# Kernel tuning notes

Measured on AMD Instinct MI355X. Metric: run time of the kernel, lower is better.

The kernel has to match this reference:

```python
import jax, jax.numpy as jnp
import numpy as np

N = 100_000   # num destination nodes (adj rows)
M = 100_000   # num source/neighbor nodes (adj cols)
E = 3_200_000 # num edges (avg degree 32)
D_IN = 128
DIM = 128
LEAKY_ALPHA = 0.2  # tf.nn.leaky_relu default


def setup_inputs() -> dict:
    key = jax.random.key(0)
    ks = jax.random.split(key, 7)
    return {
        "self_embedding": jax.random.normal(ks[0], (N, D_IN), jnp.float32),
        "neigh_embedding": jax.random.normal(ks[1], (M, D_IN), jnp.float32),
        "W": jax.random.normal(ks[2], (D_IN, DIM), jnp.float32) / np.sqrt(D_IN).astype(np.float32),
        "w_self": jax.random.normal(ks[3], (DIM, 1), jnp.float32) * 0.1,
        "w_neigh": jax.random.normal(ks[4], (DIM, 1), jnp.float32) * 0.1,
        "edge_row": jax.random.randint(ks[5], (E,), 0, N, jnp.int32),
        "edge_col": jax.random.randint(ks[6], (E,), 0, M, jnp.int32),
    }


def reference(self_embedding, neigh_embedding, W, w_self, w_neigh, edge_row, edge_col):
    # Dense projections (shared weight, no bias)
    from_all = neigh_embedding @ W    # [M, DIM]
    from_self = self_embedding @ W    # [N, DIM]

    # Per-node attention logits
    self_weight = (from_self @ w_self)[:, 0]   # [N]
    all_weight = (from_all @ w_neigh)[:, 0]    # [M]

    # Per-edge score: leaky_relu(self_weight[row] + all_weight[col])
    scores = jax.nn.leaky_relu(self_weight[edge_row] + all_weight[edge_col],
                               negative_slope=LEAKY_ALPHA)  # [E]

    n = self_embedding.shape[0]
    # Sparse (segment) softmax over each row's edges, numerically stable
    row_max = jax.ops.segment_max(scores, edge_row, num_segments=n)
    row_max = jnp.where(jnp.isfinite(row_max), row_max, 0.0)  # guard empty rows
    e = jnp.exp(scores - row_max[edge_row])
    denom = jax.ops.segment_sum(e, edge_row, num_segments=n)
    denom = jnp.where(denom > 0, denom, 1.0)
    alpha = e / denom[edge_row]  # [E]

    # Sparse-dense matmul: output[i] = sum_j alpha_ij * from_all[j]
    agg = jax.ops.segment_sum(alpha[:, None] * from_all[edge_col], edge_row,
                              num_segments=n)  # [N, DIM]

    # renorm=False path: residual with from_self, then activation
    return jax.nn.relu(from_self + agg)
```

## Files before the change

### kernel.cpp

```cpp
#include <hip/hip_runtime.h>
#include <math.h>

#define DIM 128
#define LEAKY 0.2f
#define CAP 80
#define RPB 128
#define NBMAX 1024
#define PART_CHUNK 4096

typedef __attribute__((ext_vector_type(8))) short short8_t;
typedef __attribute__((ext_vector_type(8))) __bf16 bf16x8;
typedef __attribute__((ext_vector_type(4))) float f32x4;

__device__ __forceinline__ unsigned short f32_to_bf16_bits(float x) {
  unsigned u = __float_as_uint(x);
  u += 0x7fffu + ((u >> 16) & 1u);
  return (unsigned short)(u >> 16);
}

__global__ __launch_bounds__(256) void gemm_neigh_q(
    const float* __restrict__ emb, const float* __restrict__ W,
    const float* __restrict__ wvec, unsigned char* __restrict__ fa_i8,
    float* __restrict__ scales, float* __restrict__ wout, int nrows)
{
  __shared__ __align__(16) char smem[34816];
  unsigned short* Wt = (unsigned short*)smem;
  int t = threadIdx.x;
  int lane = t & 63;
  int wid = t >> 6;

  for (int i = t; i < 4096; i += 256) {
    int k = i >> 5;
    int c4 = (i & 31) << 2;
    float4 w4 = *(const float4*)(W + k * 128 + c4);
    Wt[(c4 + 0) * 136 + k] = f32_to_bf16_bits(w4.x);
    Wt[(c4 + 1) * 136 + k] = f32_to_bf16_bits(w4.y);
    Wt[(c4 + 2) * 136 + k] = f32_to_bf16_bits(w4.z);
    Wt[(c4 + 3) * 136 + k] = f32_to_bf16_bits(w4.w);
  }
  __syncthreads();

  int row0 = blockIdx.x * 128 + wid * 32;
  bool active = row0 < nrows;
  int lr = lane & 15;
  int lk = lane >> 4;

  f32x4 acc[2][8];
  if (active) {
    bf16x8 a[2][4];
#pragma unroll
    for (int rf = 0; rf < 2; rf++) {
      int row = row0 + rf * 16 + lr;
      row = min(row, nrows - 1);
      const float* src = emb + (size_t)row * DIM;
#pragma unroll
      for (int ks = 0; ks < 4; ks++) {
        int kb = ks * 32 + lk * 8;
        float4 x = *(const float4*)(src + kb);
        float4 y = *(const float4*)(src + kb + 4);
        union { short8_t s; bf16x8 b; } f;
        f.s[0] = (short)f32_to_bf16_bits(x.x); f.s[1] = (short)f32_to_bf16_bits(x.y);
        f.s[2] = (short)f32_to_bf16_bits(x.z); f.s[3] = (short)f32_to_bf16_bits(x.w);
        f.s[4] = (short)f32_to_bf16_bits(y.x); f.s[5] = (short)f32_to_bf16_bits(y.y);
        f.s[6] = (short)f32_to_bf16_bits(y.z); f.s[7] = (short)f32_to_bf16_bits(y.w);
        a[rf][ks] = f.b;
      }
    }
#pragma unroll
    for (int rf = 0; rf < 2; rf++)
#pragma unroll
      for (int cf = 0; cf < 8; cf++)
        acc[rf][cf] = (f32x4){0.f, 0.f, 0.f, 0.f};
#pragma unroll
    for (int ks = 0; ks < 4; ks++) {
#pragma unroll
      for (int cf = 0; cf < 8; cf++) {
        bf16x8 wf = *(const bf16x8*)(Wt + (cf * 16 + lr) * 136 + ks * 32 + lk * 8);
        acc[0][cf] = __builtin_amdgcn_mfma_f32_16x16x32_bf16(a[0][ks], wf, acc[0][cf], 0, 0, 0);
        acc[1][cf] = __builtin_amdgcn_mfma_f32_16x16x32_bf16(a[1][ks], wf, acc[1][cf], 0, 0, 0);
      }
    }
  }
  __syncthreads();

  unsigned char* Q = (unsigned char*)smem + wid * 4096;
  if (active) {
#pragma unroll
    for (int rf = 0; rf < 2; rf++) {
      float pp[4] = {0.f, 0.f, 0.f, 0.f};
#pragma unroll
      for (int cf = 0; cf < 8; cf++) {
        float wvv = wvec[cf * 16 + lr];
#pragma unroll
        for (int r = 0; r < 4; r++) pp[r] += acc[rf][cf][r] * wvv;
      }
#pragma unroll
      for (int r = 0; r < 4; r++) {
        pp[r] += __shfl_xor(pp[r], 1);
        pp[r] += __shfl_xor(pp[r], 2);
        pp[r] += __shfl_xor(pp[r], 4);
        pp[r] += __shfl_xor(pp[r], 8);
      }
      float m[4];
#pragma unroll
      for (int r = 0; r < 4; r++) {
        float mm = 0.f;
#pragma unroll
        for (int cf = 0; cf < 8; cf++) mm = fmaxf(mm, fabsf(acc[rf][cf][r]));
        mm = fmaxf(mm, __shfl_xor(mm, 1));
        mm = fmaxf(mm, __shfl_xor(mm, 2));
        mm = fmaxf(mm, __shfl_xor(mm, 4));
        mm = fmaxf(mm, __shfl_xor(mm, 8));
        m[r] = mm;
      }
#pragma unroll
      for (int r = 0; r < 4; r++) {
        int rl = rf * 16 + lk * 4 + r;
        int row = row0 + rl;
        float inv = m[r] > 0.f ? 127.f / m[r] : 0.f;
        if (row < nrows && lr == 0) {
          wout[row] = pp[r];
          scales[row] = m[r] * (1.f / 127.f);
        }
#pragma unroll
        for (int cf = 0; cf < 8; cf++) {
          int q = (int)__builtin_rintf(acc[rf][cf][r] * inv) + 128;
          Q[rl * 128 + cf * 16 + lr] = (unsigned char)(q & 0xff);
        }
      }
    }
  }
  __syncthreads();

  if (active) {
    unsigned char* dstb = fa_i8 + (size_t)row0 * DIM;
    int nbytes = min(32, nrows - row0) * DIM;
    for (int i = lane * 16; i < 4096; i += 1024) {
      if (i < nbytes)
        *(uint4*)(dstb + i) = *(const uint4*)(Q + i);
    }
  }
}

__global__ __launch_bounds__(256) void gemm_self_f32(
    const float* __restrict__ emb, const float* __restrict__ W,
    const float* __restrict__ wvec, float* __restrict__ out,
    float* __restrict__ wout, int nrows)
{
  __shared__ unsigned short Wt[128 * 136];
  int t = threadIdx.x;
  int lane = t & 63;
  int wid = t >> 6;

  for (int i = t; i < 4096; i += 256) {
    int k = i >> 5;
    int c4 = (i & 31) << 2;
    float4 w4 = *(const float4*)(W + k * 128 + c4);
    Wt[(c4 + 0) * 136 + k] = f32_to_bf16_bits(w4.x);
    Wt[(c4 + 1) * 136 + k] = f32_to_bf16_bits(w4.y);
    Wt[(c4 + 2) * 136 + k] = f32_to_bf16_bits(w4.z);
    Wt[(c4 + 3) * 136 + k] = f32_to_bf16_bits(w4.w);
  }
  __syncthreads();

  int row0 = blockIdx.x * 128 + wid * 32;
  if (row0 >= nrows) return;

  int lr = lane & 15;
  int lk = lane >> 4;

  bf16x8 a[2][4];
#pragma unroll
  for (int rf = 0; rf < 2; rf++) {
    int row = row0 + rf * 16 + lr;
    row = min(row, nrows - 1);
    const float* src = emb + (size_t)row * DIM;
#pragma unroll
    for (int ks = 0; ks < 4; ks++) {
      int kb = ks * 32 + lk * 8;
      float4 x = *(const float4*)(src + kb);
      float4 y = *(const float4*)(src + kb + 4);
      union { short8_t s; bf16x8 b; } f;
      f.s[0] = (short)f32_to_bf16_bits(x.x); f.s[1] = (short)f32_to_bf16_bits(x.y);
      f.s[2] = (short)f32_to_bf16_bits(x.z); f.s[3] = (short)f32_to_bf16_bits(x.w);
      f.s[4] = (short)f32_to_bf16_bits(y.x); f.s[5] = (short)f32_to_bf16_bits(y.y);
      f.s[6] = (short)f32_to_bf16_bits(y.z); f.s[7] = (short)f32_to_bf16_bits(y.w);
      a[rf][ks] = f.b;
    }
  }

  f32x4 acc[2][8];
#pragma unroll
  for (int rf = 0; rf < 2; rf++)
#pragma unroll
    for (int cf = 0; cf < 8; cf++)
      acc[rf][cf] = (f32x4){0.f, 0.f, 0.f, 0.f};

#pragma unroll
  for (int ks = 0; ks < 4; ks++) {
#pragma unroll
    for (int cf = 0; cf < 8; cf++) {
      bf16x8 wf = *(const bf16x8*)(Wt + (cf * 16 + lr) * 136 + ks * 32 + lk * 8);
      acc[0][cf] = __builtin_amdgcn_mfma_f32_16x16x32_bf16(a[0][ks], wf, acc[0][cf], 0, 0, 0);
      acc[1][cf] = __builtin_amdgcn_mfma_f32_16x16x32_bf16(a[1][ks], wf, acc[1][cf], 0, 0, 0);
    }
  }

#pragma unroll
  for (int rf = 0; rf < 2; rf++) {
    float pp[4] = {0.f, 0.f, 0.f, 0.f};
#pragma unroll
    for (int cf = 0; cf < 8; cf++) {
      float wvv = wvec[cf * 16 + lr];
#pragma unroll
      for (int r = 0; r < 4; r++) pp[r] += acc[rf][cf][r] * wvv;
    }
#pragma unroll
    for (int r = 0; r < 4; r++) {
      pp[r] += __shfl_xor(pp[r], 1);
      pp[r] += __shfl_xor(pp[r], 2);
      pp[r] += __shfl_xor(pp[r], 4);
      pp[r] += __shfl_xor(pp[r], 8);
    }
#pragma unroll
    for (int r = 0; r < 4; r++) {
      int row = row0 + rf * 16 + lk * 4 + r;
      if (row < nrows) {
        if (lr == 0) wout[row] = pp[r];
#pragma unroll
        for (int cf = 0; cf < 8; cf++)
          out[(size_t)row * DIM + cf * 16 + lr] = acc[rf][cf][r];
      }
    }
  }
}

__global__ __launch_bounds__(256) void partition_edges(
    const int* __restrict__ erow, const int* __restrict__ ecol,
    unsigned* __restrict__ streams, int capB, int* __restrict__ gcur,
    int E, int nb)
{
  __shared__ int cnt[NBMAX];
  __shared__ int base_[NBMAX];
  __shared__ int pos[NBMAX];
  int t = threadIdx.x;
  for (int i = t; i < nb; i += 256) { cnt[i] = 0; pos[i] = 0; }
  __syncthreads();

  int e0 = blockIdx.x * PART_CHUNK + t * 16;
  int rows[16], cols[16];
#pragma unroll
  for (int q = 0; q < 4; q++) {
    int e = e0 + q * 4;
    if (e + 3 < E) {
      *(int4*)(rows + q * 4) = *(const int4*)(erow + e);
      *(int4*)(cols + q * 4) = *(const int4*)(ecol + e);
    } else {
#pragma unroll
      for (int j = 0; j < 4; j++) {
        rows[q * 4 + j] = (e + j < E) ? erow[e + j] : -1;
        cols[q * 4 + j] = (e + j < E) ? ecol[e + j] : 0;
      }
    }
  }
#pragma unroll
  for (int j = 0; j < 16; j++)
    if (rows[j] >= 0) atomicAdd(&cnt[rows[j] >> 7], 1);
  __syncthreads();
  for (int i = t; i < nb; i += 256)
    base_[i] = cnt[i] ? atomicAdd(gcur + i, cnt[i]) : 0;
  __syncthreads();
#pragma unroll
  for (int j = 0; j < 16; j++) {
    if (rows[j] >= 0) {
      int b = rows[j] >> 7;
      int idx = base_[b] + atomicAdd(&pos[b], 1);
      if (idx < capB)
        streams[(size_t)b * capB + idx] =
            (unsigned)cols[j] | ((unsigned)(rows[j] & (RPB - 1)) << 20);
    }
  }
}

__global__ __launch_bounds__(256) void scatter_aggregate(
    const unsigned* __restrict__ streams, int capB,
    const int* __restrict__ gcur,
    const unsigned char* __restrict__ fa_i8, const float* __restrict__ scales,
    const float* __restrict__ sw, const float* __restrict__ aw,
    float* __restrict__ out, int N)
{
  __shared__ __align__(16) unsigned slots[RPB * CAP];
  __shared__ int cnt[RPB];
  int b = blockIdx.x;
  int t = threadIdx.x;
  for (int i = t; i < RPB; i += 256) cnt[i] = 0;
  __syncthreads();

  int n = min(gcur[b], capB);
  const unsigned* s = streams + (size_t)b * capB;
  for (int i = t; i < n; i += 256) {
    unsigned v = s[i];
    int rl = v >> 20;
    int p = atomicAdd(&cnt[rl], 1);
    if (p < CAP) slots[rl * CAP + p] = v & 0xFFFFFu;
  }
  __syncthreads();

  int wid = t >> 6;
  int lane = t & 63;
  int g  = lane >> 3;
  int sl = lane & 7;
  int row0 = b * RPB;

  for (int rl = wid; rl < RPB; rl += 4) {
    int row = row0 + rl;
    if (row >= N) break;
    int deg = min(cnt[rl], CAP);
    float swr = sw[row];

    size_t o = (size_t)row * DIM + sl * 16;
    float4 rr0, rr1, rr2, rr3;
    if (g == 0) {
      rr0 = *(const float4*)(out + o);
      rr1 = *(const float4*)(out + o + 4);
      rr2 = *(const float4*)(out + o + 8);
      rr3 = *(const float4*)(out + o + 12);
    }

    float acc[16];
#pragma unroll
    for (int k = 0; k < 16; k++) acc[k] = 0.f;
    float dsum = 0.f, Bl = 0.f;

    for (int bb = 0; bb < deg; bb += 64) {
      int nact = min(64, deg - bb);
      int c = 0; float e = 0.f, a2 = 0.f;
      if (lane < nact) {
        c = (int)slots[rl * CAP + bb + lane];
        float v = swr + aw[c];
        v = v > 0.f ? v : LEAKY * v;
        e = __expf(v);
        a2 = e * scales[c];
      }
      dsum += e;

      for (int half = 0; half < 2; half++) {
        if (half * 32 >= nact) break;
#pragma unroll
        for (int jj = 0; jj < 4; jj++) {
          int eidx = half * 32 + (jj << 3) + g;
          float aj = __shfl(a2, eidx);
          int   cj = __shfl(c, eidx);
          uint4 u = *(const uint4*)(fa_i8 + (size_t)cj * DIM + sl * 16);
          Bl += aj;
          acc[0]  += aj * (float)( u.x        & 0xffu);
          acc[1]  += aj * (float)((u.x >> 8 ) & 0xffu);
          acc[2]  += aj * (float)((u.x >> 16) & 0xffu);
          acc[3]  += aj * (float)( u.x >> 24);
          acc[4]  += aj * (float)( u.y        & 0xffu);
          acc[5]  += aj * (float)((u.y >> 8 ) & 0xffu);
          acc[6]  += aj * (float)((u.y >> 16) & 0xffu);
          acc[7]  += aj * (float)( u.y >> 24);
          acc[8]  += aj * (float)( u.z        & 0xffu);
          acc[9]  += aj * (float)((u.z >> 8 ) & 0xffu);
          acc[10] += aj * (float)((u.z >> 16) & 0xffu);
          acc[11] += aj * (float)( u.z >> 24);
          acc[12] += aj * (float)( u.w        & 0xffu);
          acc[13] += aj * (float)((u.w >> 8 ) & 0xffu);
          acc[14] += aj * (float)((u.w >> 16) & 0xffu);
          acc[15] += aj * (float)( u.w >> 24);
        }
      }
    }

#pragma unroll
    for (int off = 32; off >= 1; off >>= 1) dsum += __shfl_xor(dsum, off);
    Bl += __shfl_xor(Bl, 8); Bl += __shfl_xor(Bl, 16); Bl += __shfl_xor(Bl, 32);
#pragma unroll
    for (int k = 0; k < 16; k++) {
      acc[k] += __shfl_xor(acc[k], 8);
      acc[k] += __shfl_xor(acc[k], 16);
      acc[k] += __shfl_xor(acc[k], 32);
    }
    float B = -128.f * Bl;
    float inv = dsum > 0.f ? 1.f / dsum : 1.f;

    if (g == 0) {
      float r[16] = {rr0.x, rr0.y, rr0.z, rr0.w, rr1.x, rr1.y, rr1.z, rr1.w,
                     rr2.x, rr2.y, rr2.z, rr2.w, rr3.x, rr3.y, rr3.z, rr3.w};
#pragma unroll
      for (int k = 0; k < 16; k++) {
        float x = r[k] + (acc[k] + B) * inv;
        r[k] = x > 0.f ? x : 0.f;
      }
      *(float4*)(out + o)      = make_float4(r[0],  r[1],  r[2],  r[3]);
      *(float4*)(out + o + 4)  = make_float4(r[4],  r[5],  r[6],  r[7]);
      *(float4*)(out + o + 8)  = make_float4(r[8],  r[9],  r[10], r[11]);
      *(float4*)(out + o + 12) = make_float4(r[12], r[13], r[14], r[15]);
    }
  }
}

extern "C" void kernel_launch(void* const* d_in, const int* in_sizes, int n_in,
                              void* d_out, int out_size, void* d_ws, size_t ws_size,
                              hipStream_t stream)
{
  const float* self_emb  = (const float*)d_in[0];
  const float* neigh_emb = (const float*)d_in[1];
  const float* W         = (const float*)d_in[2];
  const float* w_self    = (const float*)d_in[3];
  const float* w_neigh   = (const float*)d_in[4];
  const int*   erow      = (const int*)d_in[5];
  const int*   ecol      = (const int*)d_in[6];

  const int N = in_sizes[0] / DIM;
  const int M = in_sizes[1] / DIM;
  const int E = in_sizes[5];

  float* out = (float*)d_out;

  char* ws = (char*)d_ws;
  size_t off = 0;
  auto alloc = [&](size_t bytes) -> char* {
    char* p = ws + off;
    off += (bytes + 255) & ~(size_t)255;
    return p;
  };
  unsigned char* fa_i8  = (unsigned char*)alloc((size_t)M * DIM);
  float* scales = (float*)alloc((size_t)M * sizeof(float));
  float* all_w  = (float*)alloc((size_t)M * sizeof(float));
  float* self_w = (float*)alloc((size_t)N * sizeof(float));
  int*   gcur   = (int*)alloc(NBMAX * sizeof(int));

  const int nb = (N + RPB - 1) / RPB;
  const int capB = E / nb + 1024;
  unsigned* streams = (unsigned*)alloc((size_t)nb * capB * sizeof(unsigned));

  hipMemsetAsync(gcur, 0, nb * sizeof(int), stream);

  gemm_neigh_q<<<(M + 127) / 128, 256, 0, stream>>>(neigh_emb, W, w_neigh,
                                                    fa_i8, scales, all_w, M);

  gemm_self_f32<<<(N + 127) / 128, 256, 0, stream>>>(self_emb, W, w_self,
                                                     out, self_w, N);

  int pblocks = (E + PART_CHUNK - 1) / PART_CHUNK;
  partition_edges<<<pblocks, 256, 0, stream>>>(erow, ecol, streams, capB, gcur, E, nb);

  scatter_aggregate<<<nb, 256, 0, stream>>>(streams, capB, gcur, fa_i8, scales,
                                            self_w, all_w, out, N);
}
```

Measured before the change: 284.5 us.

## Split bucket scatter from aggregation into separate kernels for finer-grained row parallelism

The fused scatter+aggregate kernel becomes two kernels. The first buckets each block's edges into a per-row CSR-like array in global memory and writes the degrees. The second launches one wavefront per row to do the softmax-weighted int8 gather. The aim is better occupancy and load balance: the old design used one block of 4 waves per 128 rows, with 40KB of LDS and only about 782 blocks. The cost is an extra kernel launch plus a global write and read of the permuted edge lists.

```diff
diff --git a/kernel.cpp b/kernel.cpp
--- a/kernel.cpp
+++ b/kernel.cpp
@@ -282,12 +282,10 @@
   }
 }
 
-__global__ __launch_bounds__(256) void scatter_aggregate(
+__global__ __launch_bounds__(256) void bucket_scatter(
     const unsigned* __restrict__ streams, int capB,
-    const int* __restrict__ gcur,
-    const unsigned char* __restrict__ fa_i8, const float* __restrict__ scales,
-    const float* __restrict__ sw, const float* __restrict__ aw,
-    float* __restrict__ out, int N)
+    const int* __restrict__ gcur, unsigned* __restrict__ perm,
+    int* __restrict__ deg, int N)
 {
   __shared__ __align__(16) unsigned slots[RPB * CAP];
   __shared__ int cnt[RPB];
@@ -306,98 +304,117 @@
   }
   __syncthreads();
 
-  int wid = t >> 6;
-  int lane = t & 63;
+  int row0 = b * RPB;
+  unsigned* dst = perm + (size_t)row0 * CAP;
+  const int W4 = CAP / 4;
+  for (int i = t; i < RPB * W4; i += 256) {
+    int rl = i / W4, w = i - rl * W4;
+    if (w * 4 < min(cnt[rl], CAP))
+      *(uint4*)(dst + rl * CAP + w * 4) = *(const uint4*)(slots + rl * CAP + w * 4);
+  }
+  for (int i = t; i < RPB; i += 256) {
+    int row = row0 + i;
+    if (row < N) deg[row] = min(cnt[i], CAP);
+  }
+}
+
+__global__ __launch_bounds__(256) void aggregate_kernel(
+    const unsigned char* __restrict__ fa_i8,
+    const float* __restrict__ scales,
+    const unsigned* __restrict__ perm, const int* __restrict__ deg_arr,
+    const float* __restrict__ sw, const float* __restrict__ aw,
+    float* __restrict__ out, int n)
+{
+  int wid = threadIdx.x >> 6;
+  int lane = threadIdx.x & 63;
+  int row = blockIdx.x * 4 + wid;
+  if (row >= n) return;
+  int deg = deg_arr[row];
+  size_t base = (size_t)row * CAP;
+
   int g  = lane >> 3;
   int sl = lane & 7;
-  int row0 = b * RPB;
-
-  for (int rl = wid; rl < RPB; rl += 4) {
-    int row = row0 + rl;
-    if (row >= N) break;
-    int deg = min(cnt[rl], CAP);
-    float swr = sw[row];
-
-    size_t o = (size_t)row * DIM + sl * 16;
-    float4 rr0, rr1, rr2, rr3;
-    if (g == 0) {
-      rr0 = *(const float4*)(out + o);
-      rr1 = *(const float4*)(out + o + 4);
-      rr2 = *(const float4*)(out + o + 8);
-      rr3 = *(const float4*)(out + o + 12);
-    }
-
-    float acc[16];
-#pragma unroll
-    for (int k = 0; k < 16; k++) acc[k] = 0.f;
-    float dsum = 0.f, Bl = 0.f;
-
-    for (int bb = 0; bb < deg; bb += 64) {
-      int nact = min(64, deg - bb);
-      int c = 0; float e = 0.f, a2 = 0.f;
-      if (lane < nact) {
-        c = (int)slots[rl * CAP + bb + lane];
-        float v = swr + aw[c];
-        v = v > 0.f ? v : LEAKY * v;
-        e = __expf(v);
-        a2 = e * scales[c];
-      }
-      dsum += e;
-
-      for (int half = 0; half < 2; half++) {
-        if (half * 32 >= nact) break;
-#pragma unroll
-        for (int jj = 0; jj < 4; jj++) {
-          int eidx = half * 32 + (jj << 3) + g;
-          float aj = __shfl(a2, eidx);
-          int   cj = __shfl(c, eidx);
-          uint4 u = *(const uint4*)(fa_i8 + (size_t)cj * DIM + sl * 16);
-          Bl += aj;
-          acc[0]  += aj * (float)( u.x        & 0xffu);
-          acc[1]  += aj * (float)((u.x >> 8 ) & 0xffu);
-          acc[2]  += aj * (float)((u.x >> 16) & 0xffu);
-          acc[3]  += aj * (float)( u.x >> 24);
-          acc[4]  += aj * (float)( u.y        & 0xffu);
-          acc[5]  += aj * (float)((u.y >> 8 ) & 0xffu);
-          acc[6]  += aj * (float)((u.y >> 16) & 0xffu);
-          acc[7]  += aj * (float)( u.y >> 24);
-          acc[8]  += aj * (float)( u.z        & 0xffu);
-          acc[9]  += aj * (float)((u.z >> 8 ) & 0xffu);
-          acc[10] += aj * (float)((u.z >> 16) & 0xffu);
-          acc[11] += aj * (float)( u.z >> 24);
-          acc[12] += aj * (float)( u.w        & 0xffu);
-          acc[13] += aj * (float)((u.w >> 8 ) & 0xffu);
-          acc[14] += aj * (float)((u.w >> 16) & 0xffu);
-          acc[15] += aj * (float)( u.w >> 24);
-        }
-      }
-    }
-
-#pragma unroll
-    for (int off = 32; off >= 1; off >>= 1) dsum += __shfl_xor(dsum, off);
-    Bl += __shfl_xor(Bl, 8); Bl += __shfl_xor(Bl, 16); Bl += __shfl_xor(Bl, 32);
+
+  size_t o = (size_t)row * DIM + sl * 16;
+  float4 rr0, rr1, rr2, rr3;
+  if (g == 0) {
+    rr0 = *(const float4*)(out + o);
+    rr1 = *(const float4*)(out + o + 4);
+    rr2 = *(const float4*)(out + o + 8);
+    rr3 = *(const float4*)(out + o + 12);
+  }
+
+  float acc[16];
+#pragma unroll
+  for (int k = 0; k < 16; k++) acc[k] = 0.f;
+  float dsum = 0.f, Bl = 0.f;
+  float swr = sw[row];
+
+  for (int bb = 0; bb < deg; bb += 64) {
+    int nact = min(64, deg - bb);
+    int c = 0; float e = 0.f, a = 0.f;
+    if (lane < nact) {
+      c = (int)perm[base + bb + lane];
+      float v = swr + aw[c];
+      v = v > 0.f ? v : LEAKY * v;
+      e = __expf(v);
+      a = e * scales[c];
+    }
+    dsum += e;
+
+    for (int half = 0; half < 2; half++) {
+      if (half * 32 >= nact) break;
+#pragma unroll
+      for (int jj = 0; jj < 4; jj++) {
+        int eidx = half * 32 + (jj << 3) + g;
+        float aj = __shfl(a, eidx);
+        int   cj = __shfl(c, eidx);
+        uint4 u = *(const uint4*)(fa_i8 + (size_t)cj * DIM + sl * 16);
+        Bl += aj;
+        acc[0]  += aj * (float)( u.x        & 0xffu);
+        acc[1]  += aj * (float)((u.x >> 8 ) & 0xffu);
+        acc[2]  += aj * (float)((u.x >> 16) & 0xffu);
+        acc[3]  += aj * (float)( u.x >> 24);
+        acc[4]  += aj * (float)( u.y        & 0xffu);
+        acc[5]  += aj * (float)((u.y >> 8 ) & 0xffu);
+        acc[6]  += aj * (float)((u.y >> 16) & 0xffu);
+        acc[7]  += aj * (float)( u.y >> 24);
+        acc[8]  += aj * (float)( u.z        & 0xffu);
+        acc[9]  += aj * (float)((u.z >> 8 ) & 0xffu);
+        acc[10] += aj * (float)((u.z >> 16) & 0xffu);
+        acc[11] += aj * (float)( u.z >> 24);
+        acc[12] += aj * (float)( u.w        & 0xffu);
+        acc[13] += aj * (float)((u.w >> 8 ) & 0xffu);
+        acc[14] += aj * (float)((u.w >> 16) & 0xffu);
+        acc[15] += aj * (float)( u.w >> 24);
+      }
+    }
+  }
+
+#pragma unroll
+  for (int off = 32; off >= 1; off >>= 1) dsum += __shfl_xor(dsum, off);
+  Bl += __shfl_xor(Bl, 8); Bl += __shfl_xor(Bl, 16); Bl += __shfl_xor(Bl, 32);
+#pragma unroll
+  for (int k = 0; k < 16; k++) {
+    acc[k] += __shfl_xor(acc[k], 8);
+    acc[k] += __shfl_xor(acc[k], 16);
+    acc[k] += __shfl_xor(acc[k], 32);
+  }
+  float B = -128.f * Bl;
+  float inv = dsum > 0.f ? 1.f / dsum : 1.f;
+
+  if (g == 0) {
+    float r[16] = {rr0.x, rr0.y, rr0.z, rr0.w, rr1.x, rr1.y, rr1.z, rr1.w,
+                   rr2.x, rr2.y, rr2.z, rr2.w, rr3.x, rr3.y, rr3.z, rr3.w};
 #pragma unroll
     for (int k = 0; k < 16; k++) {
-      acc[k] += __shfl_xor(acc[k], 8);
-      acc[k] += __shfl_xor(acc[k], 16);
-      acc[k] += __shfl_xor(acc[k], 32);
-    }
-    float B = -128.f * Bl;
-    float inv = dsum > 0.f ? 1.f / dsum : 1.f;
-
-    if (g == 0) {
-      float r[16] = {rr0.x, rr0.y, rr0.z, rr0.w, rr1.x, rr1.y, rr1.z, rr1.w,
-                     rr2.x, rr2.y, rr2.z, rr2.w, rr3.x, rr3.y, rr3.z, rr3.w};
-#pragma unroll
-      for (int k = 0; k < 16; k++) {
-        float x = r[k] + (acc[k] + B) * inv;
-        r[k] = x > 0.f ? x : 0.f;
-      }
-      *(float4*)(out + o)      = make_float4(r[0],  r[1],  r[2],  r[3]);
-      *(float4*)(out + o + 4)  = make_float4(r[4],  r[5],  r[6],  r[7]);
-      *(float4*)(out + o + 8)  = make_float4(r[8],  r[9],  r[10], r[11]);
-      *(float4*)(out + o + 12) = make_float4(r[12], r[13], r[14], r[15]);
-    }
+      float x = r[k] + (acc[k] + B) * inv;
+      r[k] = x > 0.f ? x : 0.f;
+    }
+    *(float4*)(out + o)      = make_float4(r[0],  r[1],  r[2],  r[3]);
+    *(float4*)(out + o + 4)  = make_float4(r[4],  r[5],  r[6],  r[7]);
+    *(float4*)(out + o + 8)  = make_float4(r[8],  r[9],  r[10], r[11]);
+    *(float4*)(out + o + 12) = make_float4(r[12], r[13], r[14], r[15]);
   }
 }
 
@@ -430,7 +447,9 @@
   float* scales = (float*)alloc((size_t)M * sizeof(float));
   float* all_w  = (float*)alloc((size_t)M * sizeof(float));
   float* self_w = (float*)alloc((size_t)N * sizeof(float));
+  int*   deg    = (int*)alloc((size_t)N * sizeof(int));
   int*   gcur   = (int*)alloc(NBMAX * sizeof(int));
+  unsigned* perm = (unsigned*)alloc((size_t)N * CAP * sizeof(unsigned));
 
   const int nb = (N + RPB - 1) / RPB;
   const int capB = E / nb + 1024;
@@ -447,6 +466,8 @@
   int pblocks = (E + PART_CHUNK - 1) / PART_CHUNK;
   partition_edges<<<pblocks, 256, 0, stream>>>(erow, ecol, streams, capB, gcur, E, nb);
 
-  scatter_aggregate<<<nb, 256, 0, stream>>>(streams, capB, gcur, fa_i8, scales,
-                                            self_w, all_w, out, N);
-}
+  bucket_scatter<<<nb, 256, 0, stream>>>(streams, capB, gcur, perm, deg, N);
+
+  aggregate_kernel<<<(N + 3) / 4, 256, 0, stream>>>(fa_i8, scales, perm, deg,
+                                                    self_w, all_w, out, N);
+}
```

After: 242.8 us. -14.6%, faster.
